# Kernel tuning notes

Hardware: AMD Instinct MI355X
Metric: run time of the kernel (lower is better)

Reference implementation:

```python
import jax, jax.numpy as jnp
import numpy as np

B = 1024          # global batch
D = 512           # embedding_size
C = 100000        # num_classes (sum over 8 shards)
S = 64.0          # ArcFace scale
M = 0.5           # ArcFace additive angular margin
EPS = 1e-30


def setup_inputs() -> dict:
    key = jax.random.key(0)
    k1, k2, k3 = jax.random.split(key, 3)
    embeddings = jax.random.normal(k1, (B, D), dtype=jnp.float32)
    weight = jax.random.normal(k2, (C, D), dtype=jnp.float32)
    labels = jax.random.randint(k3, (B,), 0, C, dtype=jnp.int64)
    return {"embeddings": embeddings, "weight": weight, "labels": labels}


def reference(embeddings, weight, labels):
    # normalize(embeddings), normalize(weight) -> cosine logits
    ne = embeddings * jax.lax.rsqrt(jnp.sum(embeddings * embeddings, axis=1, keepdims=True))
    nw = weight * jax.lax.rsqrt(jnp.sum(weight * weight, axis=1, keepdims=True))
    logits = jnp.clip(jnp.einsum("bd,cd->bc", ne, nw), -1.0, 1.0)  # [B, C]

    rows = jnp.arange(B)
    target_logit = logits[rows, labels]
    # ArcFace: cos(theta + m), theta+m clipped to pi (insightface CombinedMarginLoss m2)
    theta = jnp.arccos(jnp.clip(target_logit, -1.0, 1.0))
    new_target = jnp.cos(jnp.minimum(theta + M, jnp.float32(np.pi)))
    logits = logits.at[rows, labels].set(new_target) * S

    # FusedDistCrossEntropy (single-device equivalent): stable softmax,
    # gather target prob, loss = -mean(log(clamp(p_target, 1e-30)))
    logp = jax.nn.log_softmax(logits, axis=1)
    p_target = jnp.exp(logp[rows, labels])
    loss = -jnp.mean(jnp.log(jnp.maximum(p_target, EPS)))
    return loss
```

## Files before the change

### kernel.cpp

```cpp
#include <hip/hip_runtime.h>
#include <hip/hip_bf16.h>
#include <math.h>
#include <stdint.h>

#define B_BATCH   1024
#define D_DIM     512
#define C_CLASSES 100000
#define BM        128
#define BN        128
#define BK        32
#define KITERS    (D_DIM / BK)
#define MTILES    (B_BATCH / BM)
#define NTILES    ((C_CLASSES + BN - 1) / BN)
#define NGROUPS   98
#define GRID_G    (8 * 8 * NGROUPS)
#define LOG2E     1.44269504088896340736f
#define COSM      0.87758256189037276f
#define SINM      0.47942553860420301f
#define NEG_LOG_EPS 69.07755278982137f

typedef short bf16x8 __attribute__((ext_vector_type(8)));
typedef float f32x4  __attribute__((ext_vector_type(4)));

static __device__ __forceinline__ unsigned short f2bf(float f) {
    unsigned int u = __builtin_bit_cast(unsigned int, f);
    u += 0x7fffu + ((u >> 16) & 1u);
    return (unsigned short)(u >> 16);
}

static __device__ __forceinline__ void gld16(const unsigned short* g, unsigned short* l) {
    __builtin_amdgcn_global_load_lds(
        (const __attribute__((address_space(1))) unsigned int*)g,
        (__attribute__((address_space(3))) unsigned int*)l, 16, 0, 0);
}

__global__ __launch_bounds__(256) void norm_embed(const float* __restrict__ E,
                                                  unsigned short* __restrict__ Abf) {
    const int b = blockIdx.x;
    const int t = threadIdx.x;
    float2 v = ((const float2*)(E + (size_t)b * D_DIM))[t];
    float ss = v.x * v.x + v.y * v.y;
    #pragma unroll
    for (int off = 1; off < 64; off <<= 1) ss += __shfl_xor(ss, off);
    __shared__ float ws4[4];
    if ((t & 63) == 0) ws4[t >> 6] = ss;
    __syncthreads();
    float inv = rsqrtf(ws4[0] + ws4[1] + ws4[2] + ws4[3]);
    unsigned int packed = (unsigned int)f2bf(v.x * inv) |
                          ((unsigned int)f2bf(v.y * inv) << 16);
    ((unsigned int*)Abf)[(size_t)b * (D_DIM / 2) + t] = packed;
}

__global__ __launch_bounds__(256) void norm_weight(const float* __restrict__ W,
                                                   unsigned short* __restrict__ Wbf) {
    const int wave = threadIdx.x >> 6;
    const int lane = threadIdx.x & 63;
    const int row = blockIdx.x * 4 + wave;
    if (row >= C_CLASSES) return;
    const float4* src = (const float4*)(W + (size_t)row * D_DIM);
    float4 v0 = src[lane];
    float4 v1 = src[lane + 64];
    float ss = v0.x*v0.x + v0.y*v0.y + v0.z*v0.z + v0.w*v0.w
             + v1.x*v1.x + v1.y*v1.y + v1.z*v1.z + v1.w*v1.w;
    #pragma unroll
    for (int off = 1; off < 64; off <<= 1) ss += __shfl_xor(ss, off);
    float inv = rsqrtf(ss);
    ushort4 o0, o1;
    o0.x = f2bf(v0.x*inv); o0.y = f2bf(v0.y*inv); o0.z = f2bf(v0.z*inv); o0.w = f2bf(v0.w*inv);
    o1.x = f2bf(v1.x*inv); o1.y = f2bf(v1.y*inv); o1.z = f2bf(v1.z*inv); o1.w = f2bf(v1.w*inv);
    ushort4* dst = (ushort4*)(Wbf + (size_t)row * D_DIM);
    dst[lane] = o0;
    dst[lane + 64] = o1;
}

static __device__ __forceinline__ float epi_term(float accv, int col, int lab,
                                                 float* __restrict__ st, int srow) {
    float c = fminf(1.f, fmaxf(-1.f, accv));
    if (col >= C_CLASSES) return 0.f;
    float s = c * 64.0f;
    if (col == lab) {
        float sn = sqrtf(fmaxf(0.f, 1.f - c * c));
        float nm = c * COSM - sn * SINM;
        if (c < -COSM) nm = -1.f;
        s = nm * 64.0f;
        st[srow] = s;
    }
    return exp2f((s - 64.0f) * LOG2E);
}

__global__ __launch_bounds__(256) void gemm_cos(const unsigned short* __restrict__ Abf,
                                                const unsigned short* __restrict__ Wbf,
                                                const int* __restrict__ labels,
                                                float* __restrict__ st,
                                                float* __restrict__ partial) {
    __shared__ unsigned short As[BM * BK];
    __shared__ unsigned short Bs[BN * BK];
    __shared__ float rowSum[BM];
    __shared__ int   labs[BM];

    const int id = blockIdx.x;
    const int x  = id & 7;
    const int s  = id >> 3;
    const int mt = s & 7;
    const int y  = x + 8 * (s >> 3);
    if (y >= NTILES) return;
    const int m0 = mt * BM;
    const int n0 = y * BN;

    const int tid = threadIdx.x;
    if (tid < BM) { labs[tid] = labels[m0 + tid]; rowSum[tid] = 0.f; }

    const int lane = tid & 63;
    const int wave = tid >> 6;
    const int wm = wave & 1, wn = wave >> 1;
    const int l15 = lane & 15, quad = lane >> 4;

    const int rsub = lane >> 2;
    const int cg   = (lane & 3) * 8;
    const int c0 = wave * 2, c1 = wave * 2 + 1;
    const unsigned short* gA0 = Abf + (size_t)(m0 + c0 * 16 + rsub) * D_DIM + cg;
    const unsigned short* gA1 = Abf + (size_t)(m0 + c1 * 16 + rsub) * D_DIM + cg;
    const int bR0 = min(n0 + c0 * 16 + rsub, C_CLASSES - 1);
    const int bR1 = min(n0 + c1 * 16 + rsub, C_CLASSES - 1);
    const unsigned short* gB0 = Wbf + (size_t)bR0 * D_DIM + cg;
    const unsigned short* gB1 = Wbf + (size_t)bR1 * D_DIM + cg;
    unsigned short* lA0 = &As[c0 * 512];
    unsigned short* lA1 = &As[c1 * 512];
    unsigned short* lB0 = &Bs[c0 * 512];
    unsigned short* lB1 = &Bs[c1 * 512];

    const f32x4 z = (f32x4){0.f, 0.f, 0.f, 0.f};
    f32x4 a00 = z, a01 = z, a02 = z, a03 = z;
    f32x4 a10 = z, a11 = z, a12 = z, a13 = z;
    f32x4 a20 = z, a21 = z, a22 = z, a23 = z;
    f32x4 a30 = z, a31 = z, a32 = z, a33 = z;

    const int aro = (wm * 64 + l15) * BK + quad * 8;
    const int bro = (wn * 64 + l15) * BK + quad * 8;

    for (int kk = 0; kk < KITERS; ++kk) {
        __syncthreads();
        gld16(gA0, lA0); gld16(gA1, lA1);
        gld16(gB0, lB0); gld16(gB1, lB1);
        gA0 += BK; gA1 += BK; gB0 += BK; gB1 += BK;
        __syncthreads();

        bf16x8 af0 = *(const bf16x8*)&As[aro];
        bf16x8 af1 = *(const bf16x8*)&As[aro + 16 * BK];
        bf16x8 af2 = *(const bf16x8*)&As[aro + 32 * BK];
        bf16x8 af3 = *(const bf16x8*)&As[aro + 48 * BK];
        bf16x8 bf0 = *(const bf16x8*)&Bs[bro];
        bf16x8 bf1 = *(const bf16x8*)&Bs[bro + 16 * BK];
        bf16x8 bf2 = *(const bf16x8*)&Bs[bro + 32 * BK];
        bf16x8 bf3 = *(const bf16x8*)&Bs[bro + 48 * BK];

        a00 = __builtin_amdgcn_mfma_f32_16x16x32_bf16(af0, bf0, a00, 0, 0, 0);
        a01 = __builtin_amdgcn_mfma_f32_16x16x32_bf16(af0, bf1, a01, 0, 0, 0);
        a02 = __builtin_amdgcn_mfma_f32_16x16x32_bf16(af0, bf2, a02, 0, 0, 0);
        a03 = __builtin_amdgcn_mfma_f32_16x16x32_bf16(af0, bf3, a03, 0, 0, 0);
        a10 = __builtin_amdgcn_mfma_f32_16x16x32_bf16(af1, bf0, a10, 0, 0, 0);
        a11 = __builtin_amdgcn_mfma_f32_16x16x32_bf16(af1, bf1, a11, 0, 0, 0);
        a12 = __builtin_amdgcn_mfma_f32_16x16x32_bf16(af1, bf2, a12, 0, 0, 0);
        a13 = __builtin_amdgcn_mfma_f32_16x16x32_bf16(af1, bf3, a13, 0, 0, 0);
        a20 = __builtin_amdgcn_mfma_f32_16x16x32_bf16(af2, bf0, a20, 0, 0, 0);
        a21 = __builtin_amdgcn_mfma_f32_16x16x32_bf16(af2, bf1, a21, 0, 0, 0);
        a22 = __builtin_amdgcn_mfma_f32_16x16x32_bf16(af2, bf2, a22, 0, 0, 0);
        a23 = __builtin_amdgcn_mfma_f32_16x16x32_bf16(af2, bf3, a23, 0, 0, 0);
        a30 = __builtin_amdgcn_mfma_f32_16x16x32_bf16(af3, bf0, a30, 0, 0, 0);
        a31 = __builtin_amdgcn_mfma_f32_16x16x32_bf16(af3, bf1, a31, 0, 0, 0);
        a32 = __builtin_amdgcn_mfma_f32_16x16x32_bf16(af3, bf2, a32, 0, 0, 0);
        a33 = __builtin_amdgcn_mfma_f32_16x16x32_bf16(af3, bf3, a33, 0, 0, 0);
    }

    const int colbase = n0 + wn * 64 + l15;

    #define EPIROW(A0, A1, A2, A3, MI)                                         \
    {                                                                          \
        _Pragma("unroll")                                                      \
        for (int r = 0; r < 4; ++r) {                                          \
            const int rloc = wm * 64 + (MI) * 16 + quad * 4 + r;               \
            const int lab = labs[rloc];                                        \
            float part = 0.f;                                                  \
            part += epi_term((A0)[r], colbase,      lab, st, m0 + rloc);       \
            part += epi_term((A1)[r], colbase + 16, lab, st, m0 + rloc);       \
            part += epi_term((A2)[r], colbase + 32, lab, st, m0 + rloc);       \
            part += epi_term((A3)[r], colbase + 48, lab, st, m0 + rloc);       \
            part += __shfl_xor(part, 1);                                       \
            part += __shfl_xor(part, 2);                                       \
            part += __shfl_xor(part, 4);                                       \
            part += __shfl_xor(part, 8);                                       \
            if (l15 == 0) atomicAdd(&rowSum[rloc], part);                      \
        }                                                                      \
    }

    EPIROW(a00, a01, a02, a03, 0)
    EPIROW(a10, a11, a12, a13, 1)
    EPIROW(a20, a21, a22, a23, 2)
    EPIROW(a30, a31, a32, a33, 3)
    #undef EPIROW

    __syncthreads();
    if (tid < BM) partial[(size_t)y * B_BATCH + m0 + tid] = rowSum[tid];
}

__global__ __launch_bounds__(64) void reduce_loss(const float* __restrict__ partial,
                                                  const float* __restrict__ st,
                                                  float* __restrict__ out) {
    const int b = blockIdx.x;
    const int l = threadIdx.x;
    float L = 0.f;
    for (int t = l; t < NTILES; t += 64) L += partial[(size_t)t * B_BATCH + b];
    #pragma unroll
    for (int off = 1; off < 64; off <<= 1) L += __shfl_xor(L, off);
    if (l == 0) {
        float logp = st[b] - 64.0f - logf(L);
        float lossb = fminf(-logp, NEG_LOG_EPS) * (1.0f / (float)B_BATCH);
        atomicAdd(out, lossb);
    }
}

extern "C" void kernel_launch(void* const* d_in, const int* in_sizes, int n_in,
                              void* d_out, int out_size, void* d_ws, size_t ws_size,
                              hipStream_t stream) {
    const float* emb = (const float*)d_in[0];
    const float* wgt = (const float*)d_in[1];
    const int*   lab = (const int*)d_in[2];
    float* out = (float*)d_out;
    char* ws = (char*)d_ws;

    const size_t WBF_B = (size_t)C_CLASSES * D_DIM * 2;
    const size_t ABF_B = (size_t)B_BATCH * D_DIM * 2;

    unsigned short* Wbf = (unsigned short*)ws;
    unsigned short* Abf = (unsigned short*)(ws + WBF_B);
    float* st      = (float*)(ws + WBF_B + ABF_B);
    float* partial = (float*)(ws + WBF_B + ABF_B + 4096);

    hipMemsetAsync(d_out, 0, sizeof(float), stream);
    norm_embed<<<B_BATCH, 256, 0, stream>>>(emb, Abf);
    norm_weight<<<(C_CLASSES + 3) / 4, 256, 0, stream>>>(wgt, Wbf);
    gemm_cos<<<GRID_G, 256, 0, stream>>>(Abf, Wbf, lab, st, partial);
    reduce_loss<<<B_BATCH, 64, 0, stream>>>(partial, st, out);
}
```

Before: 485.3 us.

## Double GEMM K-tile with XOR-swizzled LDS layout and two rows per wave in weight norm

The GEMM K tile grows from 32 to 64, which halves the number of barrier-separated load iterations. Each thread now issues four 16-byte global-to-LDS loads per operand, and the LDS column chunks are XOR-swizzled by row so the fragment reads avoid bank conflicts. The weight-normalization kernel processes two rows per wave, so each block handles eight rows and the bounds check is dropped (100000 divides by 8 evenly). In exchange the GEMM uses more LDS per block, which could lower occupancy.

```diff
diff --git a/kernel.cpp b/kernel.cpp
--- a/kernel.cpp
+++ b/kernel.cpp
@@ -8,7 +8,7 @@
 #define C_CLASSES 100000
 #define BM        128
 #define BN        128
-#define BK        32
+#define BK        64
 #define KITERS    (D_DIM / BK)
 #define MTILES    (B_BATCH / BM)
 #define NTILES    ((C_CLASSES + BN - 1) / BN)
@@ -55,22 +55,33 @@
                                                    unsigned short* __restrict__ Wbf) {
     const int wave = threadIdx.x >> 6;
     const int lane = threadIdx.x & 63;
-    const int row = blockIdx.x * 4 + wave;
-    if (row >= C_CLASSES) return;
-    const float4* src = (const float4*)(W + (size_t)row * D_DIM);
-    float4 v0 = src[lane];
-    float4 v1 = src[lane + 64];
-    float ss = v0.x*v0.x + v0.y*v0.y + v0.z*v0.z + v0.w*v0.w
-             + v1.x*v1.x + v1.y*v1.y + v1.z*v1.z + v1.w*v1.w;
+    const int row0 = blockIdx.x * 8 + wave * 2;
+    const int row1 = row0 + 1;
+    const float4* s0 = (const float4*)(W + (size_t)row0 * D_DIM);
+    const float4* s1 = (const float4*)(W + (size_t)row1 * D_DIM);
+    float4 a0 = s0[lane];
+    float4 a1 = s0[lane + 64];
+    float4 b0 = s1[lane];
+    float4 b1 = s1[lane + 64];
+    float sa = a0.x*a0.x + a0.y*a0.y + a0.z*a0.z + a0.w*a0.w
+             + a1.x*a1.x + a1.y*a1.y + a1.z*a1.z + a1.w*a1.w;
+    float sb = b0.x*b0.x + b0.y*b0.y + b0.z*b0.z + b0.w*b0.w
+             + b1.x*b1.x + b1.y*b1.y + b1.z*b1.z + b1.w*b1.w;
     #pragma unroll
-    for (int off = 1; off < 64; off <<= 1) ss += __shfl_xor(ss, off);
-    float inv = rsqrtf(ss);
-    ushort4 o0, o1;
-    o0.x = f2bf(v0.x*inv); o0.y = f2bf(v0.y*inv); o0.z = f2bf(v0.z*inv); o0.w = f2bf(v0.w*inv);
-    o1.x = f2bf(v1.x*inv); o1.y = f2bf(v1.y*inv); o1.z = f2bf(v1.z*inv); o1.w = f2bf(v1.w*inv);
-    ushort4* dst = (ushort4*)(Wbf + (size_t)row * D_DIM);
-    dst[lane] = o0;
-    dst[lane + 64] = o1;
+    for (int off = 1; off < 64; off <<= 1) {
+        sa += __shfl_xor(sa, off);
+        sb += __shfl_xor(sb, off);
+    }
+    float ia = rsqrtf(sa), ib = rsqrtf(sb);
+    ushort4 oa0, oa1, ob0, ob1;
+    oa0.x = f2bf(a0.x*ia); oa0.y = f2bf(a0.y*ia); oa0.z = f2bf(a0.z*ia); oa0.w = f2bf(a0.w*ia);
+    oa1.x = f2bf(a1.x*ia); oa1.y = f2bf(a1.y*ia); oa1.z = f2bf(a1.z*ia); oa1.w = f2bf(a1.w*ia);
+    ob0.x = f2bf(b0.x*ib); ob0.y = f2bf(b0.y*ib); ob0.z = f2bf(b0.z*ib); ob0.w = f2bf(b0.w*ib);
+    ob1.x = f2bf(b1.x*ib); ob1.y = f2bf(b1.y*ib); ob1.z = f2bf(b1.z*ib); ob1.w = f2bf(b1.w*ib);
+    ushort4* d0 = (ushort4*)(Wbf + (size_t)row0 * D_DIM);
+    ushort4* d1 = (ushort4*)(Wbf + (size_t)row1 * D_DIM);
+    d0[lane] = oa0; d0[lane + 64] = oa1;
+    d1[lane] = ob0; d1[lane + 64] = ob1;
 }
 
 static __device__ __forceinline__ float epi_term(float accv, int col, int lab,
@@ -115,19 +126,29 @@
     const int wm = wave & 1, wn = wave >> 1;
     const int l15 = lane & 15, quad = lane >> 4;
 
-    const int rsub = lane >> 2;
-    const int cg   = (lane & 3) * 8;
-    const int c0 = wave * 2, c1 = wave * 2 + 1;
-    const unsigned short* gA0 = Abf + (size_t)(m0 + c0 * 16 + rsub) * D_DIM + cg;
-    const unsigned short* gA1 = Abf + (size_t)(m0 + c1 * 16 + rsub) * D_DIM + cg;
-    const int bR0 = min(n0 + c0 * 16 + rsub, C_CLASSES - 1);
-    const int bR1 = min(n0 + c1 * 16 + rsub, C_CLASSES - 1);
-    const unsigned short* gB0 = Wbf + (size_t)bR0 * D_DIM + cg;
-    const unsigned short* gB1 = Wbf + (size_t)bR1 * D_DIM + cg;
-    unsigned short* lA0 = &As[c0 * 512];
-    unsigned short* lA1 = &As[c1 * 512];
-    unsigned short* lB0 = &Bs[c0 * 512];
-    unsigned short* lB1 = &Bs[c1 * 512];
+    const int rsub = lane >> 3;
+    const int cgsw = ((lane & 7) ^ rsub) * 8;
+    const int c0 = wave * 4;
+    const unsigned short* gA0 = Abf + (size_t)(m0 + (c0 + 0) * 8 + rsub) * D_DIM + cgsw;
+    const unsigned short* gA1 = Abf + (size_t)(m0 + (c0 + 1) * 8 + rsub) * D_DIM + cgsw;
+    const unsigned short* gA2 = Abf + (size_t)(m0 + (c0 + 2) * 8 + rsub) * D_DIM + cgsw;
+    const unsigned short* gA3 = Abf + (size_t)(m0 + (c0 + 3) * 8 + rsub) * D_DIM + cgsw;
+    const int bRa = min(n0 + (c0 + 0) * 8 + rsub, C_CLASSES - 1);
+    const int bRb = min(n0 + (c0 + 1) * 8 + rsub, C_CLASSES - 1);
+    const int bRc = min(n0 + (c0 + 2) * 8 + rsub, C_CLASSES - 1);
+    const int bRd = min(n0 + (c0 + 3) * 8 + rsub, C_CLASSES - 1);
+    const unsigned short* gB0 = Wbf + (size_t)bRa * D_DIM + cgsw;
+    const unsigned short* gB1 = Wbf + (size_t)bRb * D_DIM + cgsw;
+    const unsigned short* gB2 = Wbf + (size_t)bRc * D_DIM + cgsw;
+    const unsigned short* gB3 = Wbf + (size_t)bRd * D_DIM + cgsw;
+    unsigned short* lA0 = &As[(c0 + 0) * 512];
+    unsigned short* lA1 = &As[(c0 + 1) * 512];
+    unsigned short* lA2 = &As[(c0 + 2) * 512];
+    unsigned short* lA3 = &As[(c0 + 3) * 512];
+    unsigned short* lB0 = &Bs[(c0 + 0) * 512];
+    unsigned short* lB1 = &Bs[(c0 + 1) * 512];
+    unsigned short* lB2 = &Bs[(c0 + 2) * 512];
+    unsigned short* lB3 = &Bs[(c0 + 3) * 512];
 
     const f32x4 z = (f32x4){0.f, 0.f, 0.f, 0.f};
     f32x4 a00 = z, a01 = z, a02 = z, a03 = z;
@@ -135,24 +156,54 @@
     f32x4 a20 = z, a21 = z, a22 = z, a23 = z;
     f32x4 a30 = z, a31 = z, a32 = z, a33 = z;
 
-    const int aro = (wm * 64 + l15) * BK + quad * 8;
-    const int bro = (wn * 64 + l15) * BK + quad * 8;
+    const int axr = l15 & 7;
+    const int arow = (wm * 64 + l15) * BK;
+    const int brow = (wn * 64 + l15) * BK;
+    const int u0 = ((quad)     ^ axr) * 8;
+    const int u1 = ((4 + quad) ^ axr) * 8;
 
     for (int kk = 0; kk < KITERS; ++kk) {
         __syncthreads();
-        gld16(gA0, lA0); gld16(gA1, lA1);
-        gld16(gB0, lB0); gld16(gB1, lB1);
-        gA0 += BK; gA1 += BK; gB0 += BK; gB1 += BK;
+        gld16(gA0, lA0); gld16(gA1, lA1); gld16(gA2, lA2); gld16(gA3, lA3);
+        gld16(gB0, lB0); gld16(gB1, lB1); gld16(gB2, lB2); gld16(gB3, lB3);
+        gA0 += BK; gA1 += BK; gA2 += BK; gA3 += BK;
+        gB0 += BK; gB1 += BK; gB2 += BK; gB3 += BK;
         __syncthreads();
 
-        bf16x8 af0 = *(const bf16x8*)&As[aro];
-        bf16x8 af1 = *(const bf16x8*)&As[aro + 16 * BK];
-        bf16x8 af2 = *(const bf16x8*)&As[aro + 32 * BK];
-        bf16x8 af3 = *(const bf16x8*)&As[aro + 48 * BK];
-        bf16x8 bf0 = *(const bf16x8*)&Bs[bro];
-        bf16x8 bf1 = *(const bf16x8*)&Bs[bro + 16 * BK];
-        bf16x8 bf2 = *(const bf16x8*)&Bs[bro + 32 * BK];
-        bf16x8 bf3 = *(const bf16x8*)&Bs[bro + 48 * BK];
+        bf16x8 af0 = *(const bf16x8*)&As[arow + u0];
+        bf16x8 af1 = *(const bf16x8*)&As[arow + 16 * BK + u0];
+        bf16x8 af2 = *(const bf16x8*)&As[arow + 32 * BK + u0];
+        bf16x8 af3 = *(const bf16x8*)&As[arow + 48 * BK + u0];
+        bf16x8 bf0 = *(const bf16x8*)&Bs[brow + u0];
+        bf16x8 bf1 = *(const bf16x8*)&Bs[brow + 16 * BK + u0];
+        bf16x8 bf2 = *(const bf16x8*)&Bs[brow + 32 * BK + u0];
+        bf16x8 bf3 = *(const bf16x8*)&Bs[brow + 48 * BK + u0];
+
+        a00 = __builtin_amdgcn_mfma_f32_16x16x32_bf16(af0, bf0, a00, 0, 0, 0);
+        a01 = __builtin_amdgcn_mfma_f32_16x16x32_bf16(af0, bf1, a01, 0, 0, 0);
+        a02 = __builtin_amdgcn_mfma_f32_16x16x32_bf16(af0, bf2, a02, 0, 0, 0);
+        a03 = __builtin_amdgcn_mfma_f32_16x16x32_bf16(af0, bf3, a03, 0, 0, 0);
+        a10 = __builtin_amdgcn_mfma_f32_16x16x32_bf16(af1, bf0, a10, 0, 0, 0);
+        a11 = __builtin_amdgcn_mfma_f32_16x16x32_bf16(af1, bf1, a11, 0, 0, 0);
+        a12 = __builtin_amdgcn_mfma_f32_16x16x32_bf16(af1, bf2, a12, 0, 0, 0);
+        a13 = __builtin_amdgcn_mfma_f32_16x16x32_bf16(af1, bf3, a13, 0, 0, 0);
+        a20 = __builtin_amdgcn_mfma_f32_16x16x32_bf16(af2, bf0, a20, 0, 0, 0);
+        a21 = __builtin_amdgcn_mfma_f32_16x16x32_bf16(af2, bf1, a21, 0, 0, 0);
+        a22 = __builtin_amdgcn_mfma_f32_16x16x32_bf16(af2, bf2, a22, 0, 0, 0);
+        a23 = __builtin_amdgcn_mfma_f32_16x16x32_bf16(af2, bf3, a23, 0, 0, 0);
+        a30 = __builtin_amdgcn_mfma_f32_16x16x32_bf16(af3, bf0, a30, 0, 0, 0);
+        a31 = __builtin_amdgcn_mfma_f32_16x16x32_bf16(af3, bf1, a31, 0, 0, 0);
+        a32 = __builtin_amdgcn_mfma_f32_16x16x32_bf16(af3, bf2, a32, 0, 0, 0);
+        a33 = __builtin_amdgcn_mfma_f32_16x16x32_bf16(af3, bf3, a33, 0, 0, 0);
+
+        af0 = *(const bf16x8*)&As[arow + u1];
+        af1 = *(const bf16x8*)&As[arow + 16 * BK + u1];
+        af2 = *(const bf16x8*)&As[arow + 32 * BK + u1];
+        af3 = *(const bf16x8*)&As[arow + 48 * BK + u1];
+        bf0 = *(const bf16x8*)&Bs[brow + u1];
+        bf1 = *(const bf16x8*)&Bs[brow + 16 * BK + u1];
+        bf2 = *(const bf16x8*)&Bs[brow + 32 * BK + u1];
+        bf3 = *(const bf16x8*)&Bs[brow + 48 * BK + u1];
 
         a00 = __builtin_amdgcn_mfma_f32_16x16x32_bf16(af0, bf0, a00, 0, 0, 0);
         a01 = __builtin_amdgcn_mfma_f32_16x16x32_bf16(af0, bf1, a01, 0, 0, 0);
@@ -238,7 +289,7 @@
 
     hipMemsetAsync(d_out, 0, sizeof(float), stream);
     norm_embed<<<B_BATCH, 256, 0, stream>>>(emb, Abf);
-    norm_weight<<<(C_CLASSES + 3) / 4, 256, 0, stream>>>(wgt, Wbf);
+    norm_weight<<<C_CLASSES / 8, 256, 0, stream>>>(wgt, Wbf);
     gemm_cos<<<GRID_G, 256, 0, stream>>>(Abf, Wbf, lab, st, partial);
     reduce_loss<<<B_BATCH, 64, 0, stream>>>(partial, st, out);
 }
```

New measurement: 519.0 us. +6.9%, slower.

## Switch normalized operands to FP8 and use FP8 MFMA with swizzled LDS

Applied to the files above, without the earlier changes.

Normalized embeddings and weights are now quantized to FP8 instead of bf16, which halves the intermediate weight buffer traffic and lets the GEMM use the FP8 MFMA instruction. BK doubles to 64 so each LDS tile covers twice the reduction depth, and an XOR swizzle is added to the LDS layout to avoid bank conflicts. norm_weight now processes two rows per wave. FP8 precision on cosine logits scaled by 64 risks accuracy loss in the softmax and loss.

```diff
diff --git a/kernel.cpp b/kernel.cpp
--- a/kernel.cpp
+++ b/kernel.cpp
@@ -8,7 +8,7 @@
 #define C_CLASSES 100000
 #define BM        128
 #define BN        128
-#define BK        32
+#define BK        64
 #define KITERS    (D_DIM / BK)
 #define MTILES    (B_BATCH / BM)
 #define NTILES    ((C_CLASSES + BN - 1) / BN)
@@ -19,23 +19,23 @@
 #define SINM      0.47942553860420301f
 #define NEG_LOG_EPS 69.07755278982137f
 
-typedef short bf16x8 __attribute__((ext_vector_type(8)));
-typedef float f32x4  __attribute__((ext_vector_type(4)));
-
-static __device__ __forceinline__ unsigned short f2bf(float f) {
-    unsigned int u = __builtin_bit_cast(unsigned int, f);
-    u += 0x7fffu + ((u >> 16) & 1u);
-    return (unsigned short)(u >> 16);
-}
-
-static __device__ __forceinline__ void gld16(const unsigned short* g, unsigned short* l) {
+typedef float f32x4 __attribute__((ext_vector_type(4)));
+typedef long long i64t;
+
+static __device__ __forceinline__ unsigned int pk4(float a, float b, float c, float d) {
+    int p = __builtin_amdgcn_cvt_pk_fp8_f32(a, b, 0, false);
+    p = __builtin_amdgcn_cvt_pk_fp8_f32(c, d, p, true);
+    return (unsigned int)p;
+}
+
+static __device__ __forceinline__ void gld16(const unsigned char* g, unsigned char* l) {
     __builtin_amdgcn_global_load_lds(
         (const __attribute__((address_space(1))) unsigned int*)g,
         (__attribute__((address_space(3))) unsigned int*)l, 16, 0, 0);
 }
 
 __global__ __launch_bounds__(256) void norm_embed(const float* __restrict__ E,
-                                                  unsigned short* __restrict__ Abf) {
+                                                  unsigned char* __restrict__ Af8) {
     const int b = blockIdx.x;
     const int t = threadIdx.x;
     float2 v = ((const float2*)(E + (size_t)b * D_DIM))[t];
@@ -46,31 +46,38 @@
     if ((t & 63) == 0) ws4[t >> 6] = ss;
     __syncthreads();
     float inv = rsqrtf(ws4[0] + ws4[1] + ws4[2] + ws4[3]);
-    unsigned int packed = (unsigned int)f2bf(v.x * inv) |
-                          ((unsigned int)f2bf(v.y * inv) << 16);
-    ((unsigned int*)Abf)[(size_t)b * (D_DIM / 2) + t] = packed;
+    int p = __builtin_amdgcn_cvt_pk_fp8_f32(v.x * inv, v.y * inv, 0, false);
+    ((unsigned short*)Af8)[(size_t)b * (D_DIM / 2) + t] = (unsigned short)(p & 0xffff);
 }
 
 __global__ __launch_bounds__(256) void norm_weight(const float* __restrict__ W,
-                                                   unsigned short* __restrict__ Wbf) {
+                                                   unsigned char* __restrict__ Wf8) {
     const int wave = threadIdx.x >> 6;
     const int lane = threadIdx.x & 63;
-    const int row = blockIdx.x * 4 + wave;
-    if (row >= C_CLASSES) return;
-    const float4* src = (const float4*)(W + (size_t)row * D_DIM);
-    float4 v0 = src[lane];
-    float4 v1 = src[lane + 64];
-    float ss = v0.x*v0.x + v0.y*v0.y + v0.z*v0.z + v0.w*v0.w
-             + v1.x*v1.x + v1.y*v1.y + v1.z*v1.z + v1.w*v1.w;
+    const int row0 = blockIdx.x * 8 + wave * 2;
+    const int row1 = row0 + 1;
+    const float4* s0 = (const float4*)(W + (size_t)row0 * D_DIM);
+    const float4* s1 = (const float4*)(W + (size_t)row1 * D_DIM);
+    float4 a0 = s0[lane];
+    float4 a1 = s0[lane + 64];
+    float4 b0 = s1[lane];
+    float4 b1 = s1[lane + 64];
+    float sa = a0.x*a0.x + a0.y*a0.y + a0.z*a0.z + a0.w*a0.w
+             + a1.x*a1.x + a1.y*a1.y + a1.z*a1.z + a1.w*a1.w;
+    float sb = b0.x*b0.x + b0.y*b0.y + b0.z*b0.z + b0.w*b0.w
+             + b1.x*b1.x + b1.y*b1.y + b1.z*b1.z + b1.w*b1.w;
     #pragma unroll
-    for (int off = 1; off < 64; off <<= 1) ss += __shfl_xor(ss, off);
-    float inv = rsqrtf(ss);
-    ushort4 o0, o1;
-    o0.x = f2bf(v0.x*inv); o0.y = f2bf(v0.y*inv); o0.z = f2bf(v0.z*inv); o0.w = f2bf(v0.w*inv);
-    o1.x = f2bf(v1.x*inv); o1.y = f2bf(v1.y*inv); o1.z = f2bf(v1.z*inv); o1.w = f2bf(v1.w*inv);
-    ushort4* dst = (ushort4*)(Wbf + (size_t)row * D_DIM);
-    dst[lane] = o0;
-    dst[lane + 64] = o1;
+    for (int off = 1; off < 64; off <<= 1) {
+        sa += __shfl_xor(sa, off);
+        sb += __shfl_xor(sb, off);
+    }
+    float ia = rsqrtf(sa), ib = rsqrtf(sb);
+    unsigned int* d0 = (unsigned int*)(Wf8 + (size_t)row0 * D_DIM);
+    unsigned int* d1 = (unsigned int*)(Wf8 + (size_t)row1 * D_DIM);
+    d0[lane]      = pk4(a0.x*ia, a0.y*ia, a0.z*ia, a0.w*ia);
+    d0[lane + 64] = pk4(a1.x*ia, a1.y*ia, a1.z*ia, a1.w*ia);
+    d1[lane]      = pk4(b0.x*ib, b0.y*ib, b0.z*ib, b0.w*ib);
+    d1[lane + 64] = pk4(b1.x*ib, b1.y*ib, b1.z*ib, b1.w*ib);
 }
 
 static __device__ __forceinline__ float epi_term(float accv, int col, int lab,
@@ -88,13 +95,13 @@
     return exp2f((s - 64.0f) * LOG2E);
 }
 
-__global__ __launch_bounds__(256) void gemm_cos(const unsigned short* __restrict__ Abf,
-                                                const unsigned short* __restrict__ Wbf,
+__global__ __launch_bounds__(256) void gemm_cos(const unsigned char* __restrict__ Af8,
+                                                const unsigned char* __restrict__ Wf8,
                                                 const int* __restrict__ labels,
                                                 float* __restrict__ st,
                                                 float* __restrict__ partial) {
-    __shared__ unsigned short As[BM * BK];
-    __shared__ unsigned short Bs[BN * BK];
+    __shared__ unsigned char As[BM * BK];
+    __shared__ unsigned char Bs[BN * BK];
     __shared__ float rowSum[BM];
     __shared__ int   labs[BM];
 
@@ -116,18 +123,18 @@
     const int l15 = lane & 15, quad = lane >> 4;
 
     const int rsub = lane >> 2;
-    const int cg   = (lane & 3) * 8;
-    const int c0 = wave * 2, c1 = wave * 2 + 1;
-    const unsigned short* gA0 = Abf + (size_t)(m0 + c0 * 16 + rsub) * D_DIM + cg;
-    const unsigned short* gA1 = Abf + (size_t)(m0 + c1 * 16 + rsub) * D_DIM + cg;
+    const int swcol = (((lane & 3) ^ (rsub & 3)) * 16);
+    const int c0 = wave * 2, c1 = c0 + 1;
+    const unsigned char* gA0 = Af8 + (size_t)(m0 + c0 * 16 + rsub) * D_DIM + swcol;
+    const unsigned char* gA1 = Af8 + (size_t)(m0 + c1 * 16 + rsub) * D_DIM + swcol;
     const int bR0 = min(n0 + c0 * 16 + rsub, C_CLASSES - 1);
     const int bR1 = min(n0 + c1 * 16 + rsub, C_CLASSES - 1);
-    const unsigned short* gB0 = Wbf + (size_t)bR0 * D_DIM + cg;
-    const unsigned short* gB1 = Wbf + (size_t)bR1 * D_DIM + cg;
-    unsigned short* lA0 = &As[c0 * 512];
-    unsigned short* lA1 = &As[c1 * 512];
-    unsigned short* lB0 = &Bs[c0 * 512];
-    unsigned short* lB1 = &Bs[c1 * 512];
+    const unsigned char* gB0 = Wf8 + (size_t)bR0 * D_DIM + swcol;
+    const unsigned char* gB1 = Wf8 + (size_t)bR1 * D_DIM + swcol;
+    unsigned char* lA0 = &As[c0 * 1024];
+    unsigned char* lA1 = &As[c1 * 1024];
+    unsigned char* lB0 = &Bs[c0 * 1024];
+    unsigned char* lB1 = &Bs[c1 * 1024];
 
     const f32x4 z = (f32x4){0.f, 0.f, 0.f, 0.f};
     f32x4 a00 = z, a01 = z, a02 = z, a03 = z;
@@ -135,8 +142,11 @@
     f32x4 a20 = z, a21 = z, a22 = z, a23 = z;
     f32x4 a30 = z, a31 = z, a32 = z, a33 = z;
 
-    const int aro = (wm * 64 + l15) * BK + quad * 8;
-    const int bro = (wn * 64 + l15) * BK + quad * 8;
+    const int sw  = (l15 & 3) << 1;
+    const int arow = (wm * 64 + l15) * BK;
+    const int brow = (wn * 64 + l15) * BK;
+    const int off0 = ((quad)     ^ sw) * 8;
+    const int off1 = ((4 + quad) ^ sw) * 8;
 
     for (int kk = 0; kk < KITERS; ++kk) {
         __syncthreads();
@@ -145,31 +155,57 @@
         gA0 += BK; gA1 += BK; gB0 += BK; gB1 += BK;
         __syncthreads();
 
-        bf16x8 af0 = *(const bf16x8*)&As[aro];
-        bf16x8 af1 = *(const bf16x8*)&As[aro + 16 * BK];
-        bf16x8 af2 = *(const bf16x8*)&As[aro + 32 * BK];
-        bf16x8 af3 = *(const bf16x8*)&As[aro + 48 * BK];
-        bf16x8 bf0 = *(const bf16x8*)&Bs[bro];
-        bf16x8 bf1 = *(const bf16x8*)&Bs[bro + 16 * BK];
-        bf16x8 bf2 = *(const bf16x8*)&Bs[bro + 32 * BK];
-        bf16x8 bf3 = *(const bf16x8*)&Bs[bro + 48 * BK];
-
-        a00 = __builtin_amdgcn_mfma_f32_16x16x32_bf16(af0, bf0, a00, 0, 0, 0);
-        a01 = __builtin_amdgcn_mfma_f32_16x16x32_bf16(af0, bf1, a01, 0, 0, 0);
-        a02 = __builtin_amdgcn_mfma_f32_16x16x32_bf16(af0, bf2, a02, 0, 0, 0);
-        a03 = __builtin_amdgcn_mfma_f32_16x16x32_bf16(af0, bf3, a03, 0, 0, 0);
-        a10 = __builtin_amdgcn_mfma_f32_16x16x32_bf16(af1, bf0, a10, 0, 0, 0);
-        a11 = __builtin_amdgcn_mfma_f32_16x16x32_bf16(af1, bf1, a11, 0, 0, 0);
-        a12 = __builtin_amdgcn_mfma_f32_16x16x32_bf16(af1, bf2, a12, 0, 0, 0);
-        a13 = __builtin_amdgcn_mfma_f32_16x16x32_bf16(af1, bf3, a13, 0, 0, 0);
-        a20 = __builtin_amdgcn_mfma_f32_16x16x32_bf16(af2, bf0, a20, 0, 0, 0);
-        a21 = __builtin_amdgcn_mfma_f32_16x16x32_bf16(af2, bf1, a21, 0, 0, 0);
-        a22 = __builtin_amdgcn_mfma_f32_16x16x32_bf16(af2, bf2, a22, 0, 0, 0);
-        a23 = __builtin_amdgcn_mfma_f32_16x16x32_bf16(af2, bf3, a23, 0, 0, 0);
-        a30 = __builtin_amdgcn_mfma_f32_16x16x32_bf16(af3, bf0, a30, 0, 0, 0);
-        a31 = __builtin_amdgcn_mfma_f32_16x16x32_bf16(af3, bf1, a31, 0, 0, 0);
-        a32 = __builtin_amdgcn_mfma_f32_16x16x32_bf16(af3, bf2, a32, 0, 0, 0);
-        a33 = __builtin_amdgcn_mfma_f32_16x16x32_bf16(af3, bf3, a33, 0, 0, 0);
+        i64t af0 = *(const i64t*)&As[arow + off0];
+        i64t af1 = *(const i64t*)&As[arow + 16 * BK + off0];
+        i64t af2 = *(const i64t*)&As[arow + 32 * BK + off0];
+        i64t af3 = *(const i64t*)&As[arow + 48 * BK + off0];
+        i64t bf0 = *(const i64t*)&Bs[brow + off0];
+        i64t bf1 = *(const i64t*)&Bs[brow + 16 * BK + off0];
+        i64t bf2 = *(const i64t*)&Bs[brow + 32 * BK + off0];
+        i64t bf3 = *(const i64t*)&Bs[brow + 48 * BK + off0];
+
+        a00 = __builtin_amdgcn_mfma_f32_16x16x32_fp8_fp8(af0, bf0, a00, 0, 0, 0);
+        a01 = __builtin_amdgcn_mfma_f32_16x16x32_fp8_fp8(af0, bf1, a01, 0, 0, 0);
+        a02 = __builtin_amdgcn_mfma_f32_16x16x32_fp8_fp8(af0, bf2, a02, 0, 0, 0);
+        a03 = __builtin_amdgcn_mfma_f32_16x16x32_fp8_fp8(af0, bf3, a03, 0, 0, 0);
+        a10 = __builtin_amdgcn_mfma_f32_16x16x32_fp8_fp8(af1, bf0, a10, 0, 0, 0);
+        a11 = __builtin_amdgcn_mfma_f32_16x16x32_fp8_fp8(af1, bf1, a11, 0, 0, 0);
+        a12 = __builtin_amdgcn_mfma_f32_16x16x32_fp8_fp8(af1, bf2, a12, 0, 0, 0);
+        a13 = __builtin_amdgcn_mfma_f32_16x16x32_fp8_fp8(af1, bf3, a13, 0, 0, 0);
+        a20 = __builtin_amdgcn_mfma_f32_16x16x32_fp8_fp8(af2, bf0, a20, 0, 0, 0);
+        a21 = __builtin_amdgcn_mfma_f32_16x16x32_fp8_fp8(af2, bf1, a21, 0, 0, 0);
+        a22 = __builtin_amdgcn_mfma_f32_16x16x32_fp8_fp8(af2, bf2, a22, 0, 0, 0);
+        a23 = __builtin_amdgcn_mfma_f32_16x16x32_fp8_fp8(af2, bf3, a23, 0, 0, 0);
+        a30 = __builtin_amdgcn_mfma_f32_16x16x32_fp8_fp8(af3, bf0, a30, 0, 0, 0);
+        a31 = __builtin_amdgcn_mfma_f32_16x16x32_fp8_fp8(af3, bf1, a31, 0, 0, 0);
+        a32 = __builtin_amdgcn_mfma_f32_16x16x32_fp8_fp8(af3, bf2, a32, 0, 0, 0);
+        a33 = __builtin_amdgcn_mfma_f32_16x16x32_fp8_fp8(af3, bf3, a33, 0, 0, 0);
+
+        af0 = *(const i64t*)&As[arow + off1];
+        af1 = *(const i64t*)&As[arow + 16 * BK + off1];
+        af2 = *(const i64t*)&As[arow + 32 * BK + off1];
+        af3 = *(const i64t*)&As[arow + 48 * BK + off1];
+        bf0 = *(const i64t*)&Bs[brow + off1];
+        bf1 = *(const i64t*)&Bs[brow + 16 * BK + off1];
+        bf2 = *(const i64t*)&Bs[brow + 32 * BK + off1];
+        bf3 = *(const i64t*)&Bs[brow + 48 * BK + off1];
+
+        a00 = __builtin_amdgcn_mfma_f32_16x16x32_fp8_fp8(af0, bf0, a00, 0, 0, 0);
+        a01 = __builtin_amdgcn_mfma_f32_16x16x32_fp8_fp8(af0, bf1, a01, 0, 0, 0);
+        a02 = __builtin_amdgcn_mfma_f32_16x16x32_fp8_fp8(af0, bf2, a02, 0, 0, 0);
+        a03 = __builtin_amdgcn_mfma_f32_16x16x32_fp8_fp8(af0, bf3, a03, 0, 0, 0);
+        a10 = __builtin_amdgcn_mfma_f32_16x16x32_fp8_fp8(af1, bf0, a10, 0, 0, 0);
+        a11 = __builtin_amdgcn_mfma_f32_16x16x32_fp8_fp8(af1, bf1, a11, 0, 0, 0);
+        a12 = __builtin_amdgcn_mfma_f32_16x16x32_fp8_fp8(af1, bf2, a12, 0, 0, 0);
+        a13 = __builtin_amdgcn_mfma_f32_16x16x32_fp8_fp8(af1, bf3, a13, 0, 0, 0);
+        a20 = __builtin_amdgcn_mfma_f32_16x16x32_fp8_fp8(af2, bf0, a20, 0, 0, 0);
+        a21 = __builtin_amdgcn_mfma_f32_16x16x32_fp8_fp8(af2, bf1, a21, 0, 0, 0);
+        a22 = __builtin_amdgcn_mfma_f32_16x16x32_fp8_fp8(af2, bf2, a22, 0, 0, 0);
+        a23 = __builtin_amdgcn_mfma_f32_16x16x32_fp8_fp8(af2, bf3, a23, 0, 0, 0);
+        a30 = __builtin_amdgcn_mfma_f32_16x16x32_fp8_fp8(af3, bf0, a30, 0, 0, 0);
+        a31 = __builtin_amdgcn_mfma_f32_16x16x32_fp8_fp8(af3, bf1, a31, 0, 0, 0);
+        a32 = __builtin_amdgcn_mfma_f32_16x16x32_fp8_fp8(af3, bf2, a32, 0, 0, 0);
+        a33 = __builtin_amdgcn_mfma_f32_16x16x32_fp8_fp8(af3, bf3, a33, 0, 0, 0);
     }
 
     const int colbase = n0 + wn * 64 + l15;
@@ -228,17 +264,17 @@
     float* out = (float*)d_out;
     char* ws = (char*)d_ws;
 
-    const size_t WBF_B = (size_t)C_CLASSES * D_DIM * 2;
-    const size_t ABF_B = (size_t)B_BATCH * D_DIM * 2;
-
-    unsigned short* Wbf = (unsigned short*)ws;
-    unsigned short* Abf = (unsigned short*)(ws + WBF_B);
-    float* st      = (float*)(ws + WBF_B + ABF_B);
-    float* partial = (float*)(ws + WBF_B + ABF_B + 4096);
+    const size_t WF8_B = (size_t)C_CLASSES * D_DIM;
+    const size_t AF8_B = (size_t)B_BATCH * D_DIM;
+
+    unsigned char* Wf8 = (unsigned char*)ws;
+    unsigned char* Af8 = (unsigned char*)(ws + WF8_B);
+    float* st      = (float*)(ws + WF8_B + AF8_B);
+    float* partial = (float*)(ws + WF8_B + AF8_B + 4096);
 
     hipMemsetAsync(d_out, 0, sizeof(float), stream);
-    norm_embed<<<B_BATCH, 256, 0, stream>>>(emb, Abf);
-    norm_weight<<<(C_CLASSES + 3) / 4, 256, 0, stream>>>(wgt, Wbf);
-    gemm_cos<<<GRID_G, 256, 0, stream>>>(Abf, Wbf, lab, st, partial);
+    norm_embed<<<B_BATCH, 256, 0, stream>>>(emb, Af8);
+    norm_weight<<<C_CLASSES / 8, 256, 0, stream>>>(wgt, Wf8);
+    gemm_cos<<<GRID_G, 256, 0, stream>>>(Af8, Wf8, lab, st, partial);
     reduce_loss<<<B_BATCH, 64, 0, stream>>>(partial, st, out);
 }
```

Result: slower. 520.4 us (+7.2%).
